# Kernel tuning notes

Measured on AMD Instinct MI355X. Metric: run time of the kernel, lower is better.

The kernel has to match this reference:

```python
import jax, jax.numpy as jnp
import numpy as np

V = 32000   # vocab
D = 1024    # dim
H = 16      # query heads
HKV = 8     # kv heads (GQA)
DH = D // H # head dim = 64
L = 2       # layers
FF = 3584   # expert hidden dim
E = 8       # experts
K = 2       # top-k
EPS = 1e-5
BASE = 1000000.0
B, S = 1, 2048


def setup_inputs() -> dict:
    key = jax.random.key(0)
    ks = jax.random.split(key, 10)
    s = 0.02
    return {
        "x": jax.random.randint(ks[0], (B, S), 0, V, dtype=jnp.int64) if jax.config.jax_enable_x64 else jax.random.randint(ks[0], (B, S), 0, V),
        "emb": jax.random.normal(ks[1], (V, D), jnp.float32) * s,
        "ln_w": jnp.ones((L, D), jnp.float32),
        "ffln_w": jnp.ones((L, D), jnp.float32),
        "wq": jax.random.normal(ks[2], (L, D, H * DH), jnp.float32) * s,
        "wk": jax.random.normal(ks[3], (L, D, HKV * DH), jnp.float32) * s,
        "wv": jax.random.normal(ks[4], (L, D, HKV * DH), jnp.float32) * s,
        "wo": jax.random.normal(ks[5], (L, H * DH, D), jnp.float32) * s,
        "gate_w": jax.random.normal(ks[6], (L, E, D), jnp.float32) * s,
        "w1": jax.random.normal(ks[7], (L, E, FF, D), jnp.float32) * s,
        "w2": jax.random.normal(ks[8], (L, E, D, FF), jnp.float32) * s,
        "w3": jax.random.normal(ks[9], (L, E, FF, D), jnp.float32) * s,
        "dec_norm_w": jnp.ones((D,), jnp.float32),
    }


def rmsnorm(x, w):
    # LayerNormParameterized(use_mean=False, shift=False) == RMSNorm, pow in fp32
    xf = x.astype(jnp.float32)
    var = jnp.mean(xf * xf, axis=-1, keepdims=True)
    return ((xf * jax.lax.rsqrt(var + EPS)).astype(x.dtype)) * w


def rope(xh, pos):
    # interleaved (complex-pair) rotary embedding, xh: [B, S, h, DH]
    half = DH // 2
    freqs = 1.0 / (BASE ** (jnp.arange(0, half, dtype=jnp.float32) * 2.0 / DH))
    ang = pos[:, None] * freqs[None, :]                       # [S, half]
    cos = jnp.cos(ang)[None, :, None, :]
    sin = jnp.sin(ang)[None, :, None, :]
    x1 = xh[..., 0::2]
    x2 = xh[..., 1::2]
    out = jnp.stack([x1 * cos - x2 * sin, x1 * sin + x2 * cos], axis=-1)
    return out.reshape(xh.shape)


def reference(x, emb, ln_w, ffln_w, wq, wk, wv, wo, gate_w, w1, w2, w3, dec_norm_w):
    h = emb[x]                                                # [B, S, D]
    pos = jnp.arange(S, dtype=jnp.float32)
    causal = jnp.tril(jnp.ones((S, S), bool))[None, None]     # [1,1,S,S]
    scale = 1.0 / np.sqrt(DH).astype(np.float32)
    for i in range(L):
        # --- attention sub-layer ---
        res = h
        xn = rmsnorm(h, ln_w[i])
        q = rope((xn @ wq[i]).reshape(B, S, H, DH), pos)
        k = rope((xn @ wk[i]).reshape(B, S, HKV, DH), pos)
        v = (xn @ wv[i]).reshape(B, S, HKV, DH)
        rep = H // HKV
        k = jnp.repeat(k, rep, axis=2)                        # [B,S,H,DH]
        v = jnp.repeat(v, rep, axis=2)
        scores = jnp.einsum('bqhd,bkhd->bhqk', q, k) * scale
        scores = jnp.where(causal, scores, jnp.float32(-1e9))
        att = jax.nn.softmax(scores, axis=-1)
        o = jnp.einsum('bhqk,bkhd->bqhd', att, v).reshape(B, S, H * DH) @ wo[i]
        h = res + o
        # --- MoE FFN sub-layer ---
        res = h
        xn = rmsnorm(h, ffln_w[i]).reshape(B * S, D)          # [T, D]
        logits = xn @ gate_w[i].T                             # [T, E]
        gates = jax.nn.softmax(logits, axis=-1)
        topw, topi = jax.lax.top_k(gates, K)                  # [T, K]
        topw = topw / jnp.sum(topw, axis=-1, keepdims=True)
        # dense combine weights [T, E] (zero for unselected experts)
        cw = jnp.einsum('tk,tke->te', topw, jax.nn.one_hot(topi, E, dtype=topw.dtype))
        y = jnp.zeros_like(xn)
        for e in range(E):                                    # fixed small expert loop
            ye = (jax.nn.silu(xn @ w1[i, e].T) * (xn @ w3[i, e].T)) @ w2[i, e].T
            y = y + cw[:, e:e + 1] * ye
        h = res + y.reshape(B, S, D)
    return rmsnorm(h, dec_norm_w)
```

## Files before the change

### kernel.cpp

```cpp
#include <hip/hip_runtime.h>

using u16 = unsigned short;
using u32 = unsigned int;

#define TT 2048
#define DM 1024
#define NH 16
#define NKV 8
#define DHD 64
#define FFD 3584
#define NE 8

typedef __bf16 bf16x8 __attribute__((ext_vector_type(8)));
typedef float f32x4 __attribute__((ext_vector_type(4)));

__device__ __forceinline__ u16 f2bf(float x){
  return __builtin_bit_cast(u16, (__bf16)x);
}
__device__ __forceinline__ float bf2f(u16 h){
  return (float)__builtin_bit_cast(__bf16, h);
}
__device__ __forceinline__ f32x4 mfma16(bf16x8 a, bf16x8 b, f32x4 c){
  return __builtin_amdgcn_mfma_f32_16x16x32_bf16(a, b, c, 0, 0, 0);
}
__device__ __forceinline__ uint4 packhi8v(float4 a, float4 b){
  u16 h0=f2bf(a.x),h1=f2bf(a.y),h2=f2bf(a.z),h3=f2bf(a.w);
  u16 h4=f2bf(b.x),h5=f2bf(b.y),h6=f2bf(b.z),h7=f2bf(b.w);
  return make_uint4((u32)h0|((u32)h1<<16),(u32)h2|((u32)h3<<16),
                    (u32)h4|((u32)h5<<16),(u32)h6|((u32)h7<<16));
}
__device__ __forceinline__ uint4 packlo8v(float4 a, float4 b){
  u16 l0=f2bf(a.x-bf2f(f2bf(a.x))),l1=f2bf(a.y-bf2f(f2bf(a.y)));
  u16 l2=f2bf(a.z-bf2f(f2bf(a.z))),l3=f2bf(a.w-bf2f(f2bf(a.w)));
  u16 l4=f2bf(b.x-bf2f(f2bf(b.x))),l5=f2bf(b.y-bf2f(f2bf(b.y)));
  u16 l6=f2bf(b.z-bf2f(f2bf(b.z))),l7=f2bf(b.w-bf2f(f2bf(b.w)));
  return make_uint4((u32)l0|((u32)l1<<16),(u32)l2|((u32)l3<<16),
                    (u32)l4|((u32)l5<<16),(u32)l6|((u32)l7<<16));
}

#define SWC(r,c) ((((c) ^ ((((r)>>1) ^ ((r)>>3)) & 3))) * 8)

__global__ __launch_bounds__(256) void k_embed(const int* __restrict__ x,
    const float* __restrict__ emb, float* __restrict__ h){
  int t = blockIdx.x;
  int d = threadIdx.x * 4;
  float4 v = *reinterpret_cast<const float4*>(emb + (size_t)x[t] * DM + d);
  *reinterpret_cast<float4*>(h + (size_t)t * DM + d) = v;
}

template<int OUTF32>
__global__ __launch_bounds__(256) void k_rmsnorm(const float* __restrict__ in,
    const float* __restrict__ w, u16* __restrict__ oh, u16* __restrict__ ol,
    float* __restrict__ of){
  int t = blockIdx.x;
  int d4 = threadIdx.x * 4;
  float4 xv = *reinterpret_cast<const float4*>(in + (size_t)t * DM + d4);
  float ss = xv.x*xv.x + xv.y*xv.y + xv.z*xv.z + xv.w*xv.w;
#pragma unroll
  for (int m = 1; m < 64; m <<= 1) ss += __shfl_xor(ss, m);
  __shared__ float sred[4];
  if ((threadIdx.x & 63) == 0) sred[threadIdx.x >> 6] = ss;
  __syncthreads();
  float tot = sred[0] + sred[1] + sred[2] + sred[3];
  float r = 1.0f / sqrtf(tot * (1.0f / DM) + 1e-5f);
  float vv[4] = {xv.x, xv.y, xv.z, xv.w};
#pragma unroll
  for (int jj = 0; jj < 4; jj++){
    float xn = (vv[jj] * r) * w[d4 + jj];
    size_t a = (size_t)t * DM + d4 + jj;
    if constexpr (OUTF32){
      of[a] = xn;
    } else {
      u16 hi = f2bf(xn);
      oh[a] = hi;
      ol[a] = f2bf(xn - bf2f(hi));
    }
  }
}

template<int NHD>
__global__ __launch_bounds__(256) void k_rope(const float* __restrict__ in,
    u16* __restrict__ oh, u16* __restrict__ ol){
  int idx = blockIdx.x * 256 + threadIdx.x;
  int j = idx & 31;
  int hd = (idx >> 5) % NHD;
  int s = idx / (32 * NHD);
  size_t base = ((size_t)s * NHD + hd) * 64 + 2 * j;
  float x1 = in[base], x2 = in[base + 1];
  float xe = (float)j * 0.03125f;
  float yf = (float)pow(1.0e6, (double)xe);
  float fr = 1.0f / yf;
  float ang = (float)s * fr;
  double ad = (double)ang;
  float c  = (float)cos(ad);
  float sn = (float)sin(ad);
  float o1 = x1 * c - x2 * sn;
  float o2 = x1 * sn + x2 * c;
  u16 h1 = f2bf(o1), h2 = f2bf(o2);
  oh[base]     = h1; ol[base]     = f2bf(o1 - bf2f(h1));
  oh[base + 1] = h2; ol[base + 1] = f2bf(o2 - bf2f(h2));
}

__global__ __launch_bounds__(256) void k_splitbuf(const float* __restrict__ in,
    u16* __restrict__ oh, u16* __restrict__ ol, int n){
  int i = blockIdx.x * 256 + threadIdx.x;
  if (i < n){
    float x = in[i];
    u16 hi = f2bf(x);
    oh[i] = hi;
    ol[i] = f2bf(x - bf2f(hi));
  }
}

__global__ __launch_bounds__(256) void k_gate(const u16* __restrict__ xh,
    const u16* __restrict__ xl, const float* __restrict__ gw,
    int* __restrict__ topi, float* __restrict__ topw, int* __restrict__ cnt){
  int wv = threadIdx.x >> 6, lane = threadIdx.x & 63;
  int t = blockIdx.x * 4 + wv;
  float x[16];
#pragma unroll
  for (int i = 0; i < 16; i++){
    size_t a = (size_t)t * DM + lane + 64 * i;
    x[i] = bf2f(xh[a]) + bf2f(xl[a]);
  }
  float lgt[8];
#pragma unroll
  for (int e = 0; e < 8; e++){
    float s = 0.f;
#pragma unroll
    for (int i = 0; i < 16; i++) s += x[i] * gw[(size_t)e * DM + lane + 64 * i];
#pragma unroll
    for (int m = 1; m < 64; m <<= 1) s += __shfl_xor(s, m);
    lgt[e] = s;
  }
  float mx = lgt[0];
#pragma unroll
  for (int e = 1; e < 8; e++) mx = fmaxf(mx, lgt[e]);
  float p[8]; float sum = 0.f;
#pragma unroll
  for (int e = 0; e < 8; e++){ p[e] = expf(lgt[e] - mx); sum += p[e]; }
  float g[8];
#pragma unroll
  for (int e = 0; e < 8; e++) g[e] = p[e] / sum;
  int t0 = 0; float b0 = g[0];
#pragma unroll
  for (int e = 1; e < 8; e++) if (g[e] > b0){ b0 = g[e]; t0 = e; }
  int t1 = -1; float b1 = -1.f;
#pragma unroll
  for (int e = 0; e < 8; e++) if (e != t0 && g[e] > b1){ b1 = g[e]; t1 = e; }
  float ssum = b0 + b1;
  float w0 = b0 / ssum, w1 = b1 / ssum;
  if (lane == 0 && t < TT){
    topi[2*t] = t0; topi[2*t+1] = t1;
    topw[2*t] = w0; topw[2*t+1] = w1;
    atomicAdd(&cnt[t0], 1);
    atomicAdd(&cnt[t1], 1);
  }
}

__global__ void k_zero8(int* cnt){ if (threadIdx.x < 8) cnt[threadIdx.x] = 0; }

__global__ void k_scan(const int* __restrict__ cnt, int* __restrict__ offp, int* __restrict__ cur){
  if (threadIdx.x == 0){
    int r = 0;
    for (int e = 0; e < 8; e++){ offp[e] = r; r += cnt[e]; }
  }
  if (threadIdx.x < 8) cur[threadIdx.x] = 0;
}

__global__ __launch_bounds__(256) void k_scatter(const int* __restrict__ topi,
    const float* __restrict__ topw, const int* __restrict__ offp, int* __restrict__ cur,
    int* __restrict__ ftok, float* __restrict__ fwt){
  int t = blockIdx.x * 256 + threadIdx.x;
  if (t < TT){
#pragma unroll
    for (int j = 0; j < 2; j++){
      int e = topi[2*t + j];
      int p = atomicAdd(&cur[e], 1);
      ftok[offp[e] + p] = t;
      fwt[offp[e] + p] = topw[2*t + j];
    }
  }
}

#define GPRELOAD(S, KK) do { \
    S##Ah0 = *reinterpret_cast<const uint4*>(Ah + arowA0 + (KK)); \
    S##Ah1 = *reinterpret_cast<const uint4*>(Ah + arowA1 + (KK)); \
    if constexpr (SPLIT){ \
      S##Al0 = *reinterpret_cast<const uint4*>(Al + arowA0 + (KK)); \
      S##Al1 = *reinterpret_cast<const uint4*>(Al + arowA1 + (KK)); \
    } \
    if constexpr (BLAYOUT == 0){ \
      const float* bp_ = Bw + (size_t)(n0 + br0) * K + (KK) + cb8; \
      S##B0 = *reinterpret_cast<const float4*>(bp_); \
      S##B1 = *reinterpret_cast<const float4*>(bp_ + 4); \
      if constexpr (TN == 128){ \
        const float* bp2_ = Bw + (size_t)(n0 + br1) * K + (KK) + cb8; \
        S##B2 = *reinterpret_cast<const float4*>(bp2_); \
        S##B3 = *reinterpret_cast<const float4*>(bp2_ + 4); \
      } \
      if constexpr (DUAL){ \
        const float* bq_ = B3w + (size_t)(n0 + br0) * K + (KK) + cb8; \
        S##B2 = *reinterpret_cast<const float4*>(bq_); \
        S##B3 = *reinterpret_cast<const float4*>(bq_ + 4); \
      } \
    } else { \
      S##B0 = *reinterpret_cast<const float4*>(Bw + (size_t)((KK) + kk1) * Nq + n0 + nn1); \
      S##B1 = *reinterpret_cast<const float4*>(Bw + (size_t)((KK) + 16 + kk1) * Nq + n0 + nn1); \
    } \
  } while(0)

#define GSTORE(S) do { \
    *reinterpret_cast<uint4*>(&Ash[r0][swA0]) = S##Ah0; \
    *reinterpret_cast<uint4*>(&Ash[r1][swA1]) = S##Ah1; \
    if constexpr (SPLIT){ \
      *reinterpret_cast<uint4*>(&Asl[r0][swA0]) = S##Al0; \
      *reinterpret_cast<uint4*>(&Asl[r1][swA1]) = S##Al1; \
    } \
    if constexpr (BLAYOUT == 0){ \
      *reinterpret_cast<uint4*>(&Bh1[br0][swB0]) = packhi8v(S##B0, S##B1); \
      if constexpr (SPLIT) *reinterpret_cast<uint4*>(&Bl1[br0][swB0]) = packlo8v(S##B0, S##B1); \
      if constexpr (TN == 128){ \
        *reinterpret_cast<uint4*>(&Bh1[br1][swB1]) = packhi8v(S##B2, S##B3); \
        if constexpr (SPLIT) *reinterpret_cast<uint4*>(&Bl1[br1][swB1]) = packlo8v(S##B2, S##B3); \
      } \
      if constexpr (DUAL){ \
        *reinterpret_cast<uint4*>(&Bh3[br0][swB0]) = packhi8v(S##B2, S##B3); \
        if constexpr (SPLIT) *reinterpret_cast<uint4*>(&Bl3[br0][swB0]) = packlo8v(S##B2, S##B3); \
      } \
    } else { \
      const float* q0 = reinterpret_cast<const float*>(&S##B0); \
      const float* q1 = reinterpret_cast<const float*>(&S##B1); \
      const int ch0 = kk1 >> 3, off0 = kk1 & 7; \
      _Pragma("unroll") \
      for (int j = 0; j < 4; j++){ \
        int row = nn1 + j; \
        int c0 = SWC(row, ch0) + off0; \
        int c1 = SWC(row, ch0 + 2) + off0; \
        u16 h0 = f2bf(q0[j]); \
        Bh1[row][c0] = h0; \
        if constexpr (SPLIT) Bl1[row][c0] = f2bf(q0[j] - bf2f(h0)); \
        u16 h1 = f2bf(q1[j]); \
        Bh1[row][c1] = h1; \
        if constexpr (SPLIT) Bl1[row][c1] = f2bf(q1[j] - bf2f(h1)); \
      } \
    } \
  } while(0)

#define MFMA_PHASE() do { \
    bf16x8 af[4], afl[4]; \
    _Pragma("unroll") \
    for (int m = 0; m < 4; m++){ \
      int Ra = wr*64 + m*16 + lr; \
      int sa = SWC(Ra, lg); \
      af[m] = *reinterpret_cast<const bf16x8*>(&Ash[Ra][sa]); \
      if constexpr (SPLIT) \
        afl[m] = *reinterpret_cast<const bf16x8*>(&Asl[Ra][sa]); \
    } \
    _Pragma("unroll") \
    for (int n = 0; n < NF; n++){ \
      int Rb = wc*(TN/2) + n*16 + lr; \
      int sb = SWC(Rb, lg); \
      bf16x8 b1 = *reinterpret_cast<const bf16x8*>(&Bh1[Rb][sb]); \
      _Pragma("unroll") \
      for (int m = 0; m < 4; m++) acc[m][n] = mfma16(af[m], b1, acc[m][n]); \
      if constexpr (SPLIT){ \
        bf16x8 bl = *reinterpret_cast<const bf16x8*>(&Bl1[Rb][sb]); \
        _Pragma("unroll") \
        for (int m = 0; m < 4; m++){ \
          acc[m][n] = mfma16(af[m], bl, acc[m][n]); \
          acc[m][n] = mfma16(afl[m], b1, acc[m][n]); \
        } \
      } \
      if constexpr (DUAL){ \
        bf16x8 b3 = *reinterpret_cast<const bf16x8*>(&Bh3[Rb][sb]); \
        _Pragma("unroll") \
        for (int m = 0; m < 4; m++) acc3[m][n] = mfma16(af[m], b3, acc3[m][n]); \
        if constexpr (SPLIT){ \
          bf16x8 b3l = *reinterpret_cast<const bf16x8*>(&Bl3[Rb][sb]); \
          _Pragma("unroll") \
          for (int m = 0; m < 4; m++){ \
            acc3[m][n] = mfma16(af[m], b3l, acc3[m][n]); \
            acc3[m][n] = mfma16(afl[m], b3, acc3[m][n]); \
          } \
        } \
      } \
    } \
  } while(0)

template<int BLAYOUT, int EPI, int SPLIT, int DUAL, int TN, int KS>
__global__ __launch_bounds__(256) void k_gemm(
    const u16* __restrict__ Ah, const u16* __restrict__ Al,
    const float* __restrict__ Bw, const float* __restrict__ B3w,
    const float* __restrict__ Bw2, const float* __restrict__ Bw3,
    size_t strideB, int N, int K,
    float* __restrict__ Cf, int ldc,
    float* __restrict__ Cf2, float* __restrict__ Cf3,
    u16* __restrict__ Ch, u16* __restrict__ Cl,
    const int* __restrict__ cntp, const int* __restrict__ offp,
    const int* __restrict__ ftok, const float* __restrict__ fwt)
{
  static_assert(!(DUAL && TN != 64), "DUAL uses TN=64");
  static_assert(!(BLAYOUT == 1 && TN != 64), "BLAYOUT=1 uses TN=64");
  int cnt = TT, off = 0, ks = 0;
  if constexpr (EPI == 2 || EPI == 3){
    int e = blockIdx.z / KS;
    ks = blockIdx.z % KS;
    cnt = cntp[e]; off = offp[e];
    if ((int)blockIdx.y * 128 >= cnt) return;
    Bw += (size_t)e * strideB;
    if constexpr (DUAL) B3w += (size_t)e * strideB;
  } else if constexpr (KS > 1){
    ks = blockIdx.z;
  }
  __shared__ u16 Ash[128][32];
  __shared__ u16 Asl[SPLIT ? 128 : 1][32];
  __shared__ u16 Bh1[TN][32];
  __shared__ u16 Bl1[SPLIT ? TN : 1][32];
  __shared__ u16 Bh3[DUAL ? TN : 1][32];
  __shared__ u16 Bl3[(DUAL && SPLIT) ? TN : 1][32];

  const int tid = threadIdx.x;
  const int m0 = blockIdx.y * 128;

  int n0, Nq = N, ldq = ldc;
  float* Cq = Cf;
  if constexpr (EPI == 4){
    int bx = blockIdx.x;
    if (bx < 16){       n0 = bx * 64;        Nq = 1024; ldq = 1024; Cq = Cf;  }
    else if (bx < 24){  n0 = (bx - 16) * 64; Nq = 512;  ldq = 512;  Cq = Cf2; Bw = Bw2; }
    else {              n0 = (bx - 24) * 64; Nq = 512;  ldq = 512;  Cq = Cf3; Bw = Bw3; }
  } else {
    n0 = blockIdx.x * TN;
  }

  const int r0 = tid >> 2;
  const int r1 = r0 + 64;
  const int ca = tid & 3;
  const int ca8 = ca * 8;
  int gr0, gr1;
  {
    int g0 = m0 + r0, g1 = m0 + r1;
    if constexpr (EPI == 2){
      gr0 = ftok[off + (g0 < cnt ? g0 : cnt - 1)];
      gr1 = ftok[off + (g1 < cnt ? g1 : cnt - 1)];
    } else if constexpr (EPI == 3){
      gr0 = off + (g0 < cnt ? g0 : cnt - 1);
      gr1 = off + (g1 < cnt ? g1 : cnt - 1);
    } else {
      gr0 = g0; gr1 = g1;
    }
  }
  const size_t arowA0 = (size_t)gr0 * K + ca8;
  const size_t arowA1 = (size_t)gr1 * K + ca8;
  const int swA0 = SWC(r0, ca), swA1 = SWC(r1, ca);

  const int br0 = tid >> 2;
  const int br1 = br0 + 64;
  const int cb8 = (tid & 3) * 8;
  const int swB0 = SWC(br0, tid & 3), swB1 = SWC(br1, tid & 3);
  const int kk1 = tid >> 4;
  const int nn1 = (tid & 15) * 4;

  const int wid = tid >> 6, lane = tid & 63;
  const int wr = wid >> 1, wc = wid & 1;
  const int lr = lane & 15, lg = lane >> 4;
  constexpr int NF = TN / 32;

  f32x4 acc[4][NF];
  f32x4 acc3[DUAL ? 4 : 1][NF];
#pragma unroll
  for (int m = 0; m < 4; m++)
#pragma unroll
    for (int n = 0; n < NF; n++){
      acc[m][n] = f32x4{0.f,0.f,0.f,0.f};
      if constexpr (DUAL) acc3[m][n] = f32x4{0.f,0.f,0.f,0.f};
    }

  uint4 aAh0, aAh1, aAl0{}, aAl1{};
  float4 aB0{}, aB1{}, aB2{}, aB3{};
  uint4 bAh0, bAh1, bAl0{}, bAl1{};
  float4 bB0{}, bB1{}, bB2{}, bB3{};

  const int kbeg = ks * (K / KS);
  const int kend = kbeg + (K / KS);

  GPRELOAD(a, kbeg);
  GPRELOAD(b, kbeg + 32);
  for (int k0 = kbeg; k0 < kend; k0 += 64){
    GSTORE(a);
    __syncthreads();
    if (k0 + 64 < kend){ GPRELOAD(a, k0 + 64); }
    MFMA_PHASE();
    __syncthreads();

    GSTORE(b);
    __syncthreads();
    if (k0 + 96 < kend){ GPRELOAD(b, k0 + 96); }
    MFMA_PHASE();
    __syncthreads();
  }

#pragma unroll
  for (int m = 0; m < 4; m++)
#pragma unroll
    for (int n = 0; n < NF; n++)
#pragma unroll
      for (int r = 0; r < 4; r++){
        int row = m0 + wr*64 + m*16 + lg*4 + r;
        int col = n0 + wc*(TN/2) + n*16 + lr;
        float v = acc[m][n][r];
        if constexpr (EPI == 0){
          Cf[(size_t)row * ldc + col] = v;
        } else if constexpr (EPI == 1){
          if constexpr (KS > 1) atomicAdd(&Cf[(size_t)row * ldc + col], v);
          else                  Cf[(size_t)row * ldc + col] += v;
        } else if constexpr (EPI == 2){
          if (row < cnt){
            float a3 = acc3[m][n][r];
            float s = v / (1.0f + expf(-v));
            float y = s * a3;
            u16 hi = f2bf(y);
            size_t oa = (size_t)(off + row) * ldc + col;
            Ch[oa] = hi;
            Cl[oa] = f2bf(y - bf2f(hi));
          }
        } else if constexpr (EPI == 3){
          if (row < cnt){
            int tok = ftok[off + row];
            float wgt = fwt[off + row];
            atomicAdd(&Cf[(size_t)tok * ldc + col], wgt * v);
          }
        } else {
          if constexpr (KS > 1) atomicAdd(&Cq[(size_t)row * ldq + col], v);
          else                  Cq[(size_t)row * ldq + col] = v;
        }
      }
}

__global__ __launch_bounds__(256) void k_attn(
    const u16* __restrict__ qh, const u16* __restrict__ ql,
    const u16* __restrict__ kh, const u16* __restrict__ kl,
    const u16* __restrict__ vh, const u16* __restrict__ vl,
    u16* __restrict__ aoh, u16* __restrict__ aol)
{
  const int h  = blockIdx.y;
  const int q0 = blockIdx.x * 64;
  const int hk = h >> 1;
  const int tid = threadIdx.x;
  const int wv = tid >> 6, lane = tid & 63;
  const int lr = lane & 15, lg = lane >> 4;
  const int qw0 = q0 + wv * 16;

  __shared__ u16 Khs[32][72], Kls[32][72];
  __shared__ u16 Vhs[64][40], Vls[64][40];
  __shared__ u16 Phs[4][16][40], Pls[4][16][40];

  bf16x8 qfh[2], qfl[2];
#pragma unroll
  for (int dc = 0; dc < 2; dc++){
    size_t qa = ((size_t)(qw0 + lr) * NH + h) * 64 + dc*32 + lg*8;
    qfh[dc] = *reinterpret_cast<const bf16x8*>(qh + qa);
    qfl[dc] = *reinterpret_cast<const bf16x8*>(ql + qa);
  }
  f32x4 oacc[4];
  float mrun[4], lrun[4];
#pragma unroll
  for (int r = 0; r < 4; r++){ mrun[r] = -1e30f; lrun[r] = 0.f; }
#pragma unroll
  for (int g = 0; g < 4; g++) oacc[g] = f32x4{0.f,0.f,0.f,0.f};

  const int nt = q0 / 32 + 2;
  for (int kt = 0; kt < nt; kt++){
    int kg = kt * 32;
    {
      int kk = tid >> 3, c8 = (tid & 7) * 8;
      size_t ka = ((size_t)(kg + kk) * NKV + hk) * 64 + c8;
      *reinterpret_cast<uint4*>(&Khs[kk][c8]) = *reinterpret_cast<const uint4*>(kh + ka);
      *reinterpret_cast<uint4*>(&Kls[kk][c8]) = *reinterpret_cast<const uint4*>(kl + ka);
      uint4 v1 = *reinterpret_cast<const uint4*>(vh + ka);
      uint4 v2 = *reinterpret_cast<const uint4*>(vl + ka);
      const u16* p1 = reinterpret_cast<const u16*>(&v1);
      const u16* p2 = reinterpret_cast<const u16*>(&v2);
#pragma unroll
      for (int j = 0; j < 8; j++){ Vhs[c8 + j][kk] = p1[j]; Vls[c8 + j][kk] = p2[j]; }
    }
    __syncthreads();

    f32x4 sc[2];
    sc[0] = f32x4{0.f,0.f,0.f,0.f};
    sc[1] = f32x4{0.f,0.f,0.f,0.f};
#pragma unroll
    for (int c = 0; c < 2; c++){
#pragma unroll
      for (int dc = 0; dc < 2; dc++){
        bf16x8 bh = *reinterpret_cast<const bf16x8*>(&Khs[c*16 + lr][dc*32 + lg*8]);
        bf16x8 bl = *reinterpret_cast<const bf16x8*>(&Kls[c*16 + lr][dc*32 + lg*8]);
        sc[c] = mfma16(qfh[dc], bh, sc[c]);
        sc[c] = mfma16(qfh[dc], bl, sc[c]);
        sc[c] = mfma16(qfl[dc], bh, sc[c]);
      }
    }
    float pnew[2][4], corr[4];
#pragma unroll
    for (int r = 0; r < 4; r++){
      int row = qw0 + lg*4 + r;
      float s0 = (kg + lr      <= row) ? sc[0][r] * 0.125f : -1e30f;
      float s1 = (kg + 16 + lr <= row) ? sc[1][r] * 0.125f : -1e30f;
      float tm = fmaxf(s0, s1);
#pragma unroll
      for (int m = 1; m < 16; m <<= 1) tm = fmaxf(tm, __shfl_xor(tm, m));
      float mnew = fmaxf(mrun[r], tm);
      corr[r] = expf(mrun[r] - mnew);
      float p0 = expf(s0 - mnew);
      float p1 = expf(s1 - mnew);
      pnew[0][r] = p0; pnew[1][r] = p1;
      float sm = p0 + p1;
#pragma unroll
      for (int m = 1; m < 16; m <<= 1) sm += __shfl_xor(sm, m);
      lrun[r] = lrun[r] * corr[r] + sm;
      mrun[r] = mnew;
    }
#pragma unroll
    for (int g = 0; g < 4; g++){
      f32x4 t = oacc[g];
#pragma unroll
      for (int r = 0; r < 4; r++) t[r] *= corr[r];
      oacc[g] = t;
    }
#pragma unroll
    for (int c = 0; c < 2; c++)
#pragma unroll
      for (int r = 0; r < 4; r++){
        float p = pnew[c][r];
        u16 hi = f2bf(p);
        Phs[wv][lg*4 + r][c*16 + lr] = hi;
        Pls[wv][lg*4 + r][c*16 + lr] = f2bf(p - bf2f(hi));
      }
    asm volatile("s_waitcnt lgkmcnt(0)" ::: "memory");
    __builtin_amdgcn_sched_barrier(0);
    bf16x8 pah = *reinterpret_cast<const bf16x8*>(&Phs[wv][lr][lg*8]);
    bf16x8 pal = *reinterpret_cast<const bf16x8*>(&Pls[wv][lr][lg*8]);
#pragma unroll
    for (int g = 0; g < 4; g++){
      bf16x8 vb1 = *reinterpret_cast<const bf16x8*>(&Vhs[g*16 + lr][lg*8]);
      bf16x8 vb2 = *reinterpret_cast<const bf16x8*>(&Vls[g*16 + lr][lg*8]);
      oacc[g] = mfma16(pah, vb1, oacc[g]);
      oacc[g] = mfma16(pah, vb2, oacc[g]);
      oacc[g] = mfma16(pal, vb1, oacc[g]);
    }
    __syncthreads();
  }
#pragma unroll
  for (int g = 0; g < 4; g++)
#pragma unroll
    for (int r = 0; r < 4; r++){
      int row = qw0 + lg*4 + r;
      float v = oacc[g][r] / lrun[r];
      u16 hi = f2bf(v);
      size_t oa = ((size_t)row * NH + h) * 64 + g*16 + lr;
      aoh[oa] = hi;
      aol[oa] = f2bf(v - bf2f(hi));
    }
}

extern "C" void kernel_launch(void* const* d_in, const int* in_sizes, int n_in,
                              void* d_out, int out_size, void* d_ws, size_t ws_size,
                              hipStream_t stream){
  const int*   x     = (const int*)d_in[0];
  const float* emb   = (const float*)d_in[1];
  const float* lnw   = (const float*)d_in[2];
  const float* fflnw = (const float*)d_in[3];
  const float* wq    = (const float*)d_in[4];
  const float* wk    = (const float*)d_in[5];
  const float* wvp   = (const float*)d_in[6];
  const float* wo    = (const float*)d_in[7];
  const float* gw    = (const float*)d_in[8];
  const float* w1    = (const float*)d_in[9];
  const float* w2    = (const float*)d_in[10];
  const float* w3    = (const float*)d_in[11];
  const float* dnw   = (const float*)d_in[12];
  float* out = (float*)d_out;

  char* p = (char*)d_ws;
  auto alloc = [&](size_t bytes)->char*{
    char* r = p; p += (bytes + 255) & ~(size_t)255; return r;
  };
  float* h    = (float*)alloc((size_t)TT * DM * 4);
  float* qbuf = (float*)alloc((size_t)TT * 1024 * 4);
  float* kbuf = (float*)alloc((size_t)TT * 512 * 4);
  float* vbuf = (float*)alloc((size_t)TT * 512 * 4);
  u16* xnh = (u16*)alloc((size_t)TT * DM * 2);
  u16* xnl = (u16*)alloc((size_t)TT * DM * 2);
  u16* qhb = (u16*)alloc((size_t)TT * 1024 * 2);
  u16* qlb = (u16*)alloc((size_t)TT * 1024 * 2);
  u16* khb = (u16*)alloc((size_t)TT * 512 * 2);
  u16* klb = (u16*)alloc((size_t)TT * 512 * 2);
  u16* vhb = (u16*)alloc((size_t)TT * 512 * 2);
  u16* vlb = (u16*)alloc((size_t)TT * 512 * 2);
  u16* aoh = (u16*)alloc((size_t)TT * 1024 * 2);
  u16* aol = (u16*)alloc((size_t)TT * 1024 * 2);
  u16* acth = (u16*)alloc((size_t)2 * TT * FFD * 2);
  u16* actl = (u16*)alloc((size_t)2 * TT * FFD * 2);
  int*   topi = (int*)alloc((size_t)2 * TT * 4);
  float* topw = (float*)alloc((size_t)2 * TT * 4);
  int* cnt  = (int*)alloc(64);
  int* offe = (int*)alloc(64);
  int* cur  = (int*)alloc(64);
  int*   ftok = (int*)alloc((size_t)2 * TT * 4);
  float* fwt  = (float*)alloc((size_t)2 * TT * 4);

  k_embed<<<TT, 256, 0, stream>>>(x, emb, h);

  for (int i = 0; i < 2; i++){
    const float* wq_i = wq + (size_t)i * DM * 1024;
    const float* wk_i = wk + (size_t)i * DM * 512;
    const float* wv_i = wvp + (size_t)i * DM * 512;
    const float* wo_i = wo + (size_t)i * 1024 * DM;
    const float* w1_i = w1 + (size_t)i * NE * FFD * DM;
    const float* w2_i = w2 + (size_t)i * NE * DM * FFD;
    const float* w3_i = w3 + (size_t)i * NE * FFD * DM;

    k_rmsnorm<0><<<TT, 256, 0, stream>>>(h, lnw + i * DM, xnh, xnl, nullptr);

    hipMemsetAsync(qbuf, 0, (size_t)TT * 1024 * 4, stream);
    hipMemsetAsync(kbuf, 0, (size_t)TT * 512 * 4, stream);
    hipMemsetAsync(vbuf, 0, (size_t)TT * 512 * 4, stream);
    k_gemm<1,4,1,0,64,2><<<dim3(32,16,2), 256, 0, stream>>>(xnh, xnl,
        wq_i, nullptr, wk_i, wv_i, 0, 1024, DM,
        qbuf, 1024, kbuf, vbuf, nullptr, nullptr, nullptr, nullptr, nullptr, nullptr);

    k_rope<16><<<4096, 256, 0, stream>>>(qbuf, qhb, qlb);
    k_rope<8><<<2048, 256, 0, stream>>>(kbuf, khb, klb);
    k_splitbuf<<<4096, 256, 0, stream>>>(vbuf, vhb, vlb, TT * 512);

    k_attn<<<dim3(32,16,1), 256, 0, stream>>>(qhb, qlb, khb, klb, vhb, vlb, aoh, aol);

    k_gemm<1,1,1,0,64,2><<<dim3(16,16,2), 256, 0, stream>>>(aoh, aol,
        wo_i, nullptr, nullptr, nullptr, 0, DM, 1024,
        h, DM, nullptr, nullptr, nullptr, nullptr, nullptr, nullptr, nullptr, nullptr);

    k_rmsnorm<0><<<TT, 256, 0, stream>>>(h, fflnw + i * DM, xnh, xnl, nullptr);

    k_zero8<<<1, 64, 0, stream>>>(cnt);
    k_gate<<<TT/4, 256, 0, stream>>>(xnh, xnl, gw + (size_t)i * NE * DM, topi, topw, cnt);
    k_scan<<<1, 64, 0, stream>>>(cnt, offe, cur);
    k_scatter<<<8, 256, 0, stream>>>(topi, topw, offe, cur, ftok, fwt);

    if (i == 0){
      k_gemm<0,2,1,1,64,1><<<dim3(FFD/64,16,8), 256, 0, stream>>>(xnh, xnl,
          w1_i, w3_i, nullptr, nullptr, (size_t)FFD * DM, FFD, DM,
          nullptr, FFD, nullptr, nullptr, acth, actl, cnt, offe, ftok, fwt);
      k_gemm<0,3,1,0,128,4><<<dim3(DM/128,16,32), 256, 0, stream>>>(acth, actl,
          w2_i, nullptr, nullptr, nullptr, (size_t)DM * FFD, DM, FFD,
          h, DM, nullptr, nullptr, nullptr, nullptr, cnt, offe, ftok, fwt);
    } else {
      k_gemm<0,2,0,1,64,1><<<dim3(FFD/64,16,8), 256, 0, stream>>>(xnh, xnl,
          w1_i, w3_i, nullptr, nullptr, (size_t)FFD * DM, FFD, DM,
          nullptr, FFD, nullptr, nullptr, acth, actl, cnt, offe, ftok, fwt);
      k_gemm<0,3,0,0,128,4><<<dim3(DM/128,16,32), 256, 0, stream>>>(acth, actl,
          w2_i, nullptr, nullptr, nullptr, (size_t)DM * FFD, DM, FFD,
          h, DM, nullptr, nullptr, nullptr, nullptr, cnt, offe, ftok, fwt);
    }
  }

  k_rmsnorm<1><<<TT, 256, 0, stream>>>(h, dnw, nullptr, nullptr, out);
}
```

Measured before the change: 1.677 ms.

## Load GEMM A tiles directly to LDS with double buffering

The A operand of the generic MFMA GEMM kernel is now copied from global memory straight into shared memory with global_load_lds, into a double-buffered A tile. This replaces the register staging and explicit LDS stores. The swizzle moves to the global address side so the LDS layout stays compatible with the existing fragment reads. The main loop now steps 32 K per iteration with one barrier pair instead of two unrolled register-staged phases. The intent is to cut VGPR pressure and LDS store instructions. The risk is that the full vmcnt(0) wait now stalls on the B prefetch as well as the A copy, and the loop runs twice as many iterations.

Result: faster. 1.499 ms (-10.6%).

```diff
diff --git a/kernel.cpp b/kernel.cpp
--- a/kernel.cpp
+++ b/kernel.cpp
@@ -38,7 +38,15 @@
                     (u32)l4|((u32)l5<<16),(u32)l6|((u32)l7<<16));
 }
 
-#define SWC(r,c) ((((c) ^ ((((r)>>1) ^ ((r)>>3)) & 3))) * 8)
+#define SWZR(r) ((((r)>>1) ^ ((r)>>3)) & 3)
+#define SWC(r,c) ((((c) ^ SWZR(r))) * 8)
+
+__device__ __forceinline__ void glds16(const u16* g, u16* l){
+  __builtin_amdgcn_global_load_lds(
+      (const __attribute__((address_space(1))) void*)g,
+      (__attribute__((address_space(3))) void*)l,
+      16, 0, 0);
+}
 
 __global__ __launch_bounds__(256) void k_embed(const int* __restrict__ x,
     const float* __restrict__ emb, float* __restrict__ h){
@@ -183,54 +191,51 @@
   }
 }
 
-#define GPRELOAD(S, KK) do { \
-    S##Ah0 = *reinterpret_cast<const uint4*>(Ah + arowA0 + (KK)); \
-    S##Ah1 = *reinterpret_cast<const uint4*>(Ah + arowA1 + (KK)); \
+#define GLDSA(BUF, KK) do { \
+    glds16(Ah + gaA0 + (KK), (u16*)&Ash[BUF][awr0][0]); \
+    glds16(Ah + gaA1 + (KK), (u16*)&Ash[BUF][awr1][0]); \
     if constexpr (SPLIT){ \
-      S##Al0 = *reinterpret_cast<const uint4*>(Al + arowA0 + (KK)); \
-      S##Al1 = *reinterpret_cast<const uint4*>(Al + arowA1 + (KK)); \
+      glds16(Al + gaA0 + (KK), (u16*)&Asl[BUF][awr0][0]); \
+      glds16(Al + gaA1 + (KK), (u16*)&Asl[BUF][awr1][0]); \
     } \
+  } while(0)
+
+#define GPRELOADB(KK) do { \
     if constexpr (BLAYOUT == 0){ \
       const float* bp_ = Bw + (size_t)(n0 + br0) * K + (KK) + cb8; \
-      S##B0 = *reinterpret_cast<const float4*>(bp_); \
-      S##B1 = *reinterpret_cast<const float4*>(bp_ + 4); \
+      pB0 = *reinterpret_cast<const float4*>(bp_); \
+      pB1 = *reinterpret_cast<const float4*>(bp_ + 4); \
       if constexpr (TN == 128){ \
         const float* bp2_ = Bw + (size_t)(n0 + br1) * K + (KK) + cb8; \
-        S##B2 = *reinterpret_cast<const float4*>(bp2_); \
-        S##B3 = *reinterpret_cast<const float4*>(bp2_ + 4); \
+        pB2 = *reinterpret_cast<const float4*>(bp2_); \
+        pB3 = *reinterpret_cast<const float4*>(bp2_ + 4); \
       } \
       if constexpr (DUAL){ \
         const float* bq_ = B3w + (size_t)(n0 + br0) * K + (KK) + cb8; \
-        S##B2 = *reinterpret_cast<const float4*>(bq_); \
-        S##B3 = *reinterpret_cast<const float4*>(bq_ + 4); \
+        pB2 = *reinterpret_cast<const float4*>(bq_); \
+        pB3 = *reinterpret_cast<const float4*>(bq_ + 4); \
       } \
     } else { \
-      S##B0 = *reinterpret_cast<const float4*>(Bw + (size_t)((KK) + kk1) * Nq + n0 + nn1); \
-      S##B1 = *reinterpret_cast<const float4*>(Bw + (size_t)((KK) + 16 + kk1) * Nq + n0 + nn1); \
+      pB0 = *reinterpret_cast<const float4*>(Bw + (size_t)((KK) + kk1) * Nq + n0 + nn1); \
+      pB1 = *reinterpret_cast<const float4*>(Bw + (size_t)((KK) + 16 + kk1) * Nq + n0 + nn1); \
     } \
   } while(0)
 
-#define GSTORE(S) do { \
-    *reinterpret_cast<uint4*>(&Ash[r0][swA0]) = S##Ah0; \
-    *reinterpret_cast<uint4*>(&Ash[r1][swA1]) = S##Ah1; \
-    if constexpr (SPLIT){ \
-      *reinterpret_cast<uint4*>(&Asl[r0][swA0]) = S##Al0; \
-      *reinterpret_cast<uint4*>(&Asl[r1][swA1]) = S##Al1; \
-    } \
+#define GSTOREB() do { \
     if constexpr (BLAYOUT == 0){ \
-      *reinterpret_cast<uint4*>(&Bh1[br0][swB0]) = packhi8v(S##B0, S##B1); \
-      if constexpr (SPLIT) *reinterpret_cast<uint4*>(&Bl1[br0][swB0]) = packlo8v(S##B0, S##B1); \
+      *reinterpret_cast<uint4*>(&Bh1[br0][swB0]) = packhi8v(pB0, pB1); \
+      if constexpr (SPLIT) *reinterpret_cast<uint4*>(&Bl1[br0][swB0]) = packlo8v(pB0, pB1); \
       if constexpr (TN == 128){ \
-        *reinterpret_cast<uint4*>(&Bh1[br1][swB1]) = packhi8v(S##B2, S##B3); \
-        if constexpr (SPLIT) *reinterpret_cast<uint4*>(&Bl1[br1][swB1]) = packlo8v(S##B2, S##B3); \
+        *reinterpret_cast<uint4*>(&Bh1[br1][swB1]) = packhi8v(pB2, pB3); \
+        if constexpr (SPLIT) *reinterpret_cast<uint4*>(&Bl1[br1][swB1]) = packlo8v(pB2, pB3); \
       } \
       if constexpr (DUAL){ \
-        *reinterpret_cast<uint4*>(&Bh3[br0][swB0]) = packhi8v(S##B2, S##B3); \
-        if constexpr (SPLIT) *reinterpret_cast<uint4*>(&Bl3[br0][swB0]) = packlo8v(S##B2, S##B3); \
+        *reinterpret_cast<uint4*>(&Bh3[br0][swB0]) = packhi8v(pB2, pB3); \
+        if constexpr (SPLIT) *reinterpret_cast<uint4*>(&Bl3[br0][swB0]) = packlo8v(pB2, pB3); \
       } \
     } else { \
-      const float* q0 = reinterpret_cast<const float*>(&S##B0); \
-      const float* q1 = reinterpret_cast<const float*>(&S##B1); \
+      const float* q0 = reinterpret_cast<const float*>(&pB0); \
+      const float* q1 = reinterpret_cast<const float*>(&pB1); \
       const int ch0 = kk1 >> 3, off0 = kk1 & 7; \
       _Pragma("unroll") \
       for (int j = 0; j < 4; j++){ \
@@ -247,15 +252,15 @@
     } \
   } while(0)
 
-#define MFMA_PHASE() do { \
+#define MFMA_PHASE(CURB) do { \
     bf16x8 af[4], afl[4]; \
     _Pragma("unroll") \
     for (int m = 0; m < 4; m++){ \
       int Ra = wr*64 + m*16 + lr; \
       int sa = SWC(Ra, lg); \
-      af[m] = *reinterpret_cast<const bf16x8*>(&Ash[Ra][sa]); \
+      af[m] = *reinterpret_cast<const bf16x8*>(&Ash[CURB][Ra][sa]); \
       if constexpr (SPLIT) \
-        afl[m] = *reinterpret_cast<const bf16x8*>(&Asl[Ra][sa]); \
+        afl[m] = *reinterpret_cast<const bf16x8*>(&Asl[CURB][Ra][sa]); \
     } \
     _Pragma("unroll") \
     for (int n = 0; n < NF; n++){ \
@@ -313,8 +318,8 @@
   } else if constexpr (KS > 1){
     ks = blockIdx.z;
   }
-  __shared__ u16 Ash[128][32];
-  __shared__ u16 Asl[SPLIT ? 128 : 1][32];
+  __shared__ u16 Ash[2][128][32];
+  __shared__ u16 Asl[SPLIT ? 2 : 1][SPLIT ? 128 : 1][32];
   __shared__ u16 Bh1[TN][32];
   __shared__ u16 Bl1[SPLIT ? TN : 1][32];
   __shared__ u16 Bh3[DUAL ? TN : 1][32];
@@ -334,26 +339,32 @@
     n0 = blockIdx.x * TN;
   }
 
-  const int r0 = tid >> 2;
-  const int r1 = r0 + 64;
-  const int ca = tid & 3;
-  const int ca8 = ca * 8;
-  int gr0, gr1;
+  const int wid = tid >> 6, lane = tid & 63;
+  const int wr = wid >> 1, wc = wid & 1;
+  const int lr = lane & 15, lg = lane >> 4;
+  constexpr int NF = TN / 32;
+
+  const int awr0 = wid * 32;
+  const int awr1 = wid * 32 + 16;
+  const int rA0 = awr0 + (lane >> 2);
+  const int rA1 = awr1 + (lane >> 2);
+  const int cA0 = (lane & 3) ^ SWZR(rA0);
+  const int cA1 = (lane & 3) ^ SWZR(rA1);
+  int grA0, grA1;
   {
-    int g0 = m0 + r0, g1 = m0 + r1;
+    int g0 = m0 + rA0, g1 = m0 + rA1;
     if constexpr (EPI == 2){
-      gr0 = ftok[off + (g0 < cnt ? g0 : cnt - 1)];
-      gr1 = ftok[off + (g1 < cnt ? g1 : cnt - 1)];
+      grA0 = ftok[off + (g0 < cnt ? g0 : cnt - 1)];
+      grA1 = ftok[off + (g1 < cnt ? g1 : cnt - 1)];
     } else if constexpr (EPI == 3){
-      gr0 = off + (g0 < cnt ? g0 : cnt - 1);
-      gr1 = off + (g1 < cnt ? g1 : cnt - 1);
+      grA0 = off + (g0 < cnt ? g0 : cnt - 1);
+      grA1 = off + (g1 < cnt ? g1 : cnt - 1);
     } else {
-      gr0 = g0; gr1 = g1;
-    }
-  }
-  const size_t arowA0 = (size_t)gr0 * K + ca8;
-  const size_t arowA1 = (size_t)gr1 * K + ca8;
-  const int swA0 = SWC(r0, ca), swA1 = SWC(r1, ca);
+      grA0 = g0; grA1 = g1;
+    }
+  }
+  const size_t gaA0 = (size_t)grA0 * K + cA0 * 8;
+  const size_t gaA1 = (size_t)grA1 * K + cA1 * 8;
 
   const int br0 = tid >> 2;
   const int br1 = br0 + 64;
@@ -362,11 +373,6 @@
   const int kk1 = tid >> 4;
   const int nn1 = (tid & 15) * 4;
 
-  const int wid = tid >> 6, lane = tid & 63;
-  const int wr = wid >> 1, wc = wid & 1;
-  const int lr = lane & 15, lg = lane >> 4;
-  constexpr int NF = TN / 32;
-
   f32x4 acc[4][NF];
   f32x4 acc3[DUAL ? 4 : 1][NF];
 #pragma unroll
@@ -377,28 +383,25 @@
       if constexpr (DUAL) acc3[m][n] = f32x4{0.f,0.f,0.f,0.f};
     }
 
-  uint4 aAh0, aAh1, aAl0{}, aAl1{};
-  float4 aB0{}, aB1{}, aB2{}, aB3{};
-  uint4 bAh0, bAh1, bAl0{}, bAl1{};
-  float4 bB0{}, bB1{}, bB2{}, bB3{};
+  float4 pB0{}, pB1{}, pB2{}, pB3{};
 
   const int kbeg = ks * (K / KS);
   const int kend = kbeg + (K / KS);
 
-  GPRELOAD(a, kbeg);
-  GPRELOAD(b, kbeg + 32);
-  for (int k0 = kbeg; k0 < kend; k0 += 64){
-    GSTORE(a);
-    __syncthreads();
-    if (k0 + 64 < kend){ GPRELOAD(a, k0 + 64); }
-    MFMA_PHASE();
-    __syncthreads();
-
-    GSTORE(b);
-    __syncthreads();
-    if (k0 + 96 < kend){ GPRELOAD(b, k0 + 96); }
-    MFMA_PHASE();
-    __syncthreads();
+  GLDSA(0, kbeg);
+  GPRELOADB(kbeg);
+  int cur = 0;
+  for (int k0 = kbeg; k0 < kend; k0 += 32){
+    GSTOREB();
+    asm volatile("s_waitcnt vmcnt(0) lgkmcnt(0)" ::: "memory");
+    __builtin_amdgcn_s_barrier();
+    if (k0 + 32 < kend){
+      GLDSA(cur ^ 1, k0 + 32);
+      GPRELOADB(k0 + 32);
+    }
+    MFMA_PHASE(cur);
+    __builtin_amdgcn_s_barrier();
+    cur ^= 1;
   }
 
 #pragma unroll
```
